# Kernel tuning notes

Measured on AMD Instinct MI355X. Metric: run time of the kernel, lower is better.

The kernel has to match this reference:

```python
import jax, jax.numpy as jnp
import numpy as np

B, T, HID = 2, 4096, 1024
NH, DK, DV = 8, 128, 128
CONV_K = 4
CHUNK = 64


def short_conv_silu(x, w):
    # causal depthwise conv1d, x: [B,T,D], w: [D,K]
    K = w.shape[1]
    xp = jnp.pad(x, ((0, 0), (K - 1, 0), (0, 0)))
    out = sum(xp[:, i:i + x.shape[1], :] * w[:, i] for i in range(K))
    return jax.nn.silu(out)


def hadamard_fm(x, w1, b1, w2, b2):
    # per-head feature map: Linear(x)*Linear(x), x: [B,T,H,D]
    return (jnp.einsum('bthd,ed->bthe', x, w1) + b1) * (jnp.einsum('bthd,ed->bthe', x, w2) + b2)


def chunk_linear_attn(q, k, v, scale):
    # causal linear attention via chunked scan. q,k,v: [B,T,H,D]
    Bq, Tq, H, Dk = q.shape
    Dv = v.shape[-1]
    nc = Tq // CHUNK
    q = (q * scale).reshape(Bq, nc, CHUNK, H, Dk).transpose(1, 0, 2, 3, 4)
    k = k.reshape(Bq, nc, CHUNK, H, Dk).transpose(1, 0, 2, 3, 4)
    v = v.reshape(Bq, nc, CHUNK, H, Dv).transpose(1, 0, 2, 3, 4)
    mask = jnp.tril(jnp.ones((CHUNK, CHUNK), dtype=bool))

    def step(S, inp):
        qc, kc, vc = inp  # [B,C,H,D]
        attn = jnp.einsum('bihk,bjhk->bhij', qc, kc)
        attn = jnp.where(mask, attn, 0.0)
        o = jnp.einsum('bhij,bjhv->bihv', attn, vc) + jnp.einsum('bihk,bhkv->bihv', qc, S)
        S = S + jnp.einsum('bihk,bihv->bhkv', kc, vc)
        return S, o

    S0 = jnp.zeros((Bq, H, Dk, Dv), q.dtype)
    _, o = jax.lax.scan(step, S0, (q, k, v))  # o: [nc,B,C,H,Dv]
    return o.transpose(1, 0, 2, 3, 4).reshape(Bq, Tq, H, Dv)


def setup_inputs() -> dict:
    key = jax.random.key(0)
    ks = jax.random.split(key, 16)
    s = 0.02
    inp = {
        'hidden_states': jax.random.normal(ks[0], (B, T, HID), jnp.float32),
        'wq': jax.random.normal(ks[1], (HID, HID), jnp.float32) * s,
        'wk': jax.random.normal(ks[2], (HID, HID), jnp.float32) * s,
        'wv': jax.random.normal(ks[3], (HID, HID), jnp.float32) * s,
        'wo': jax.random.normal(ks[4], (HID, HID), jnp.float32) * s,
        'conv_q': jax.random.normal(ks[5], (HID, CONV_K), jnp.float32) * 0.2,
        'conv_k': jax.random.normal(ks[6], (HID, CONV_K), jnp.float32) * 0.2,
        'conv_v': jax.random.normal(ks[7], (HID, CONV_K), jnp.float32) * 0.2,
        'fmq_w1': jax.random.normal(ks[8], (DK, DK), jnp.float32) * s,
        'fmq_b1': jnp.zeros((DK,), jnp.float32),
        'fmq_w2': jax.random.normal(ks[9], (DK, DK), jnp.float32) * s,
        'fmq_b2': jnp.zeros((DK,), jnp.float32),
        'fmk_w1': jax.random.normal(ks[10], (DK, DK), jnp.float32) * s,
        'fmk_b1': jnp.zeros((DK,), jnp.float32),
        'fmk_w2': jax.random.normal(ks[11], (DK, DK), jnp.float32) * s,
        'fmk_b2': jnp.zeros((DK,), jnp.float32),
    }
    return inp


def reference(hidden_states, wq, wk, wv, wo, conv_q, conv_k, conv_v,
              fmq_w1, fmq_b1, fmq_w2, fmq_b2, fmk_w1, fmk_b1, fmk_w2, fmk_b2):
    q = short_conv_silu(hidden_states @ wq.T, conv_q)
    k = short_conv_silu(hidden_states @ wk.T, conv_k)
    v = short_conv_silu(hidden_states @ wv.T, conv_v)
    q = q.reshape(B, T, NH, DK)
    k = k.reshape(B, T, NH, DK)
    v = v.reshape(B, T, NH, DV)
    q = hadamard_fm(q, fmq_w1, fmq_b1, fmq_w2, fmq_b2)
    k = hadamard_fm(k, fmk_w1, fmk_b1, fmk_w2, fmk_b2)
    scale = DK ** -0.5
    o = chunk_linear_attn(q, k, v, scale)
    return o.reshape(B, T, NH * DV) @ wo.T
```

## Files before the change

### kernel.cpp

```cpp
#include <hip/hip_runtime.h>
#include <cstdint>
#include <cstddef>

#define T_SEQ 4096
#define BATCH 2
#define HIDDEN 1024
#define NHEAD 8
#define DKV 128
#define BT (BATCH * T_SEQ)
#define NCH 64
#define CHUNK_L 64
#define QSCALE 0.08838834764831845f
#define SCALE_P 1024.0f
#define SCALE_O 8192.0f
#define OEPS 0.7071067811865476f

typedef _Float16 half8 __attribute__((ext_vector_type(8)));
typedef float floatx4 __attribute__((ext_vector_type(4)));

union HBits { _Float16 h; unsigned short u; };

__global__ void cast_f32_f16(const float* __restrict__ X, _Float16* __restrict__ Y, int n8)
{
    int idx = blockIdx.x * 256 + threadIdx.x;
    if (idx < n8) {
        float4 a = ((const float4*)X)[idx * 2];
        float4 b = ((const float4*)X)[idx * 2 + 1];
        half8 h = { (_Float16)a.x, (_Float16)a.y, (_Float16)a.z, (_Float16)a.w,
                    (_Float16)b.x, (_Float16)b.y, (_Float16)b.z, (_Float16)b.w };
        *(half8*)&Y[idx * 8] = h;
    }
}

__global__ void cast8_f32_f16(const float* __restrict__ s0, const float* __restrict__ s1,
                              const float* __restrict__ s2, const float* __restrict__ s3,
                              const float* __restrict__ s4, const float* __restrict__ s5,
                              const float* __restrict__ s6, const float* __restrict__ s7,
                              _Float16* __restrict__ d0, _Float16* __restrict__ d1,
                              _Float16* __restrict__ d2, _Float16* __restrict__ d3,
                              _Float16* __restrict__ d4, _Float16* __restrict__ d5,
                              _Float16* __restrict__ d6, _Float16* __restrict__ d7,
                              int nbig, int nsmall)
{
    int sel = blockIdx.y;
    const float* src; _Float16* dst; int n8;
    switch (sel) {
        case 0: src = s0; dst = d0; n8 = nbig; break;
        case 1: src = s1; dst = d1; n8 = nbig; break;
        case 2: src = s2; dst = d2; n8 = nbig; break;
        case 3: src = s3; dst = d3; n8 = nbig; break;
        case 4: src = s4; dst = d4; n8 = nsmall; break;
        case 5: src = s5; dst = d5; n8 = nsmall; break;
        case 6: src = s6; dst = d6; n8 = nsmall; break;
        default: src = s7; dst = d7; n8 = nsmall; break;
    }
    int idx = blockIdx.x * 256 + threadIdx.x;
    if (idx < n8) {
        float4 u = ((const float4*)src)[idx * 2];
        float4 v = ((const float4*)src)[idx * 2 + 1];
        half8 h = { (_Float16)u.x, (_Float16)u.y, (_Float16)u.z, (_Float16)u.w,
                    (_Float16)v.x, (_Float16)v.y, (_Float16)v.z, (_Float16)v.w };
        *(half8*)&dst[idx * 8] = h;
    }
}

__global__ __launch_bounds__(256) void gemm_nt_f16_h16(const _Float16* __restrict__ A,
                                                       const _Float16* __restrict__ W,
                                                       _Float16* __restrict__ C,
                                                       int M, int N, int K)
{
    __shared__ _Float16 As[128 * 64];
    __shared__ _Float16 Ws[128 * 64];
    const int bm = blockIdx.y * 128;
    const int bn = blockIdx.x * 128;
    const int tid = threadIdx.x;
    const int w = tid >> 6;
    const int l = tid & 63;
    const int wm = (w >> 1) * 64;
    const int wn = (w & 1) * 64;
    const int lane16 = l & 15;
    const int quad = l >> 4;
    const int srow = w * 8 + (l >> 3);
    const int skh = ((l & 7) ^ (l >> 3)) * 8;
    const int rsw = lane16 & 7;

    floatx4 acc[4][4];
#pragma unroll
    for (int i = 0; i < 4; ++i)
#pragma unroll
        for (int j = 0; j < 4; ++j)
            acc[i][j] = (floatx4){0.f, 0.f, 0.f, 0.f};

    for (int k0 = 0; k0 < K; k0 += 64) {
#pragma unroll
        for (int c = 0; c < 4; ++c) {
            int row = c * 32 + srow;
            const _Float16* ga = A + (size_t)(bm + row) * K + k0 + skh;
            const _Float16* gw = W + (size_t)(bn + row) * K + k0 + skh;
            __builtin_amdgcn_global_load_lds(
                (const __attribute__((address_space(1))) void*)ga,
                (__attribute__((address_space(3))) void*)(As + c * 2048 + w * 512), 16, 0, 0);
            __builtin_amdgcn_global_load_lds(
                (const __attribute__((address_space(1))) void*)gw,
                (__attribute__((address_space(3))) void*)(Ws + c * 2048 + w * 512), 16, 0, 0);
        }
        __syncthreads();

#pragma unroll
        for (int s = 0; s < 2; ++s) {
            const int pc = (((s * 4 + quad) ^ rsw)) * 8;
            half8 a[4], b[4];
#pragma unroll
            for (int i = 0; i < 4; ++i) {
                a[i] = *(const half8*)&As[(wm + i * 16 + lane16) * 64 + pc];
                b[i] = *(const half8*)&Ws[(wn + i * 16 + lane16) * 64 + pc];
            }
#pragma unroll
            for (int i = 0; i < 4; ++i)
#pragma unroll
                for (int j = 0; j < 4; ++j)
                    acc[i][j] = __builtin_amdgcn_mfma_f32_16x16x32_f16(a[i], b[j], acc[i][j], 0, 0, 0);
        }
        __syncthreads();
    }
#pragma unroll
    for (int i = 0; i < 4; ++i)
#pragma unroll
        for (int j = 0; j < 4; ++j)
#pragma unroll
            for (int r = 0; r < 4; ++r)
                C[(size_t)(bm + wm + i * 16 + quad * 4 + r) * N + bn + wn + j * 16 + lane16] =
                    (_Float16)acc[i][j][r];
}

__global__ __launch_bounds__(256) void gemm_nt_f16_f32(const _Float16* __restrict__ A,
                                                       const _Float16* __restrict__ W,
                                                       float* __restrict__ C,
                                                       int M, int N, int K, float scale)
{
    __shared__ _Float16 As[128 * 64];
    __shared__ _Float16 Ws[128 * 64];
    const int bm = blockIdx.y * 128;
    const int bn = blockIdx.x * 128;
    const int tid = threadIdx.x;
    const int w = tid >> 6;
    const int l = tid & 63;
    const int wm = (w >> 1) * 64;
    const int wn = (w & 1) * 64;
    const int lane16 = l & 15;
    const int quad = l >> 4;
    const int srow = w * 8 + (l >> 3);
    const int skh = ((l & 7) ^ (l >> 3)) * 8;
    const int rsw = lane16 & 7;

    floatx4 acc[4][4];
#pragma unroll
    for (int i = 0; i < 4; ++i)
#pragma unroll
        for (int j = 0; j < 4; ++j)
            acc[i][j] = (floatx4){0.f, 0.f, 0.f, 0.f};

    for (int k0 = 0; k0 < K; k0 += 64) {
#pragma unroll
        for (int c = 0; c < 4; ++c) {
            int row = c * 32 + srow;
            const _Float16* ga = A + (size_t)(bm + row) * K + k0 + skh;
            const _Float16* gw = W + (size_t)(bn + row) * K + k0 + skh;
            __builtin_amdgcn_global_load_lds(
                (const __attribute__((address_space(1))) void*)ga,
                (__attribute__((address_space(3))) void*)(As + c * 2048 + w * 512), 16, 0, 0);
            __builtin_amdgcn_global_load_lds(
                (const __attribute__((address_space(1))) void*)gw,
                (__attribute__((address_space(3))) void*)(Ws + c * 2048 + w * 512), 16, 0, 0);
        }
        __syncthreads();

#pragma unroll
        for (int s = 0; s < 2; ++s) {
            const int pc = (((s * 4 + quad) ^ rsw)) * 8;
            half8 a[4], b[4];
#pragma unroll
            for (int i = 0; i < 4; ++i) {
                a[i] = *(const half8*)&As[(wm + i * 16 + lane16) * 64 + pc];
                b[i] = *(const half8*)&Ws[(wn + i * 16 + lane16) * 64 + pc];
            }
#pragma unroll
            for (int i = 0; i < 4; ++i)
#pragma unroll
                for (int j = 0; j < 4; ++j)
                    acc[i][j] = __builtin_amdgcn_mfma_f32_16x16x32_f16(a[i], b[j], acc[i][j], 0, 0, 0);
        }
        __syncthreads();
    }
#pragma unroll
    for (int i = 0; i < 4; ++i)
#pragma unroll
        for (int j = 0; j < 4; ++j)
#pragma unroll
            for (int r = 0; r < 4; ++r)
                C[(size_t)(bm + wm + i * 16 + quad * 4 + r) * N + bn + wn + j * 16 + lane16] =
                    acc[i][j][r] * scale;
}

__global__ __launch_bounds__(256) void conv_silu_T(const _Float16* __restrict__ X, int ldx,
                                                   const float* __restrict__ Wc,
                                                   _Float16* __restrict__ VT)
{
    __shared__ _Float16 xs[67 * 64];
    const int bx = blockIdx.x;
    const int t0 = (bx & 63) * 64;
    const int dt = ((bx >> 6) & 15) * 64;
    const int z = bx >> 10;
    const int tid = threadIdx.x;

#pragma unroll
    for (int i = 0; i < 3; ++i) {
        int p = tid + 256 * i;
        if (p < 536) {
            int row = p >> 3, d8 = (p & 7) * 8;
            int t = t0 - 3 + row;
            half8 v;
            if (t >= 0)
                v = *(const half8*)&X[((size_t)z * T_SEQ + t) * ldx + dt + d8];
            else
                v = (half8){0, 0, 0, 0, 0, 0, 0, 0};
            *(half8*)&xs[row * 64 + d8] = v;
        }
    }
    __syncthreads();

    const int d = tid & 63;
    const int dg = dt + d;
    float4 w = *(const float4*)&Wc[dg * 4];
#pragma unroll
    for (int u = 0; u < 2; ++u) {
        int tg = (tid >> 6) + u * 4;
        half8 o;
#pragma unroll
        for (int s = 0; s < 8; ++s) {
            int base = (tg * 8 + s + 3) * 64 + d;
            float acc = (float)xs[base] * w.w
                      + (float)xs[base - 64] * w.z
                      + (float)xs[base - 128] * w.y
                      + (float)xs[base - 192] * w.x;
            o[s] = (_Float16)(acc / (1.f + __expf(-acc)));
        }
        *(half8*)&VT[((size_t)z * HIDDEN + dg) * T_SEQ + t0 + tg * 8] = o;
    }
}

#define XIN_LD 136
__global__ __launch_bounds__(256) void convfm(const _Float16* __restrict__ QKV, int ldx,
                                              const float* __restrict__ Wcq,
                                              const float* __restrict__ Wck,
                                              const _Float16* __restrict__ Wfm,
                                              const float* __restrict__ Bq1,
                                              const float* __restrict__ Bq2,
                                              const float* __restrict__ Bk1,
                                              const float* __restrict__ Bk2,
                                              _Float16* __restrict__ OUTq,
                                              _Float16* __restrict__ OUTk)
{
    const int sel = blockIdx.z;
    const float* Wc = sel ? Wck : Wcq;
    const _Float16* W1h = Wfm + (sel ? 2 * 16384 : 0);
    const _Float16* W2h = Wfm + (sel ? 3 * 16384 : 16384);
    const float* B1 = sel ? Bk1 : Bq1;
    const float* B2 = sel ? Bk2 : Bq2;
    _Float16* OUT = sel ? OUTk : OUTq;

    __shared__ _Float16 xin[67 * XIN_LD];
    __shared__ _Float16 xs[4 * 64 * 32];
    const int t0 = blockIdx.x * 64;
    const int h = blockIdx.y;
    const int tid = threadIdx.x;
    const int w = tid >> 6;
    const int l = tid & 63;
    const int lane16 = l & 15;
    const int quad = l >> 4;
    const bool batch_start = (t0 & (T_SEQ - 1)) == 0;

    for (int p = tid; p < 67 * 16; p += 256) {
        int row = p >> 4, cg = p & 15;
        half8 v;
        if (batch_start && row < 3)
            v = (half8){0, 0, 0, 0, 0, 0, 0, 0};
        else
            v = *(const half8*)&QKV[(size_t)(t0 - 3 + row) * ldx + sel * HIDDEN + h * DKV + cg * 8];
        *(half8*)&xin[row * XIN_LD + cg * 8] = v;
    }
    __syncthreads();

    {
        const int doct = tid & 15;
        const int d0 = doct * 8;
        const int rq = (tid >> 4) * 4;
        const int u = doct >> 2;
        const int col = d0 & 31;

        float w0[8], w1[8], w2[8], w3[8];
#pragma unroll
        for (int e = 0; e < 8; ++e) {
            float4 wv = *(const float4*)&Wc[(h * DKV + d0 + e) * 4];
            w0[e] = wv.x; w1[e] = wv.y; w2[e] = wv.z; w3[e] = wv.w;
        }

#pragma unroll
        for (int rr = 0; rr < 4; ++rr) {
            const int row = rq + rr;
            half8 x3 = *(const half8*)&xin[(row + 0) * XIN_LD + d0];
            half8 x2 = *(const half8*)&xin[(row + 1) * XIN_LD + d0];
            half8 x1 = *(const half8*)&xin[(row + 2) * XIN_LD + d0];
            half8 x0 = *(const half8*)&xin[(row + 3) * XIN_LD + d0];
            half8 o;
#pragma unroll
            for (int e = 0; e < 8; ++e) {
                float acc = fmaf((float)x0[e], w3[e],
                            fmaf((float)x1[e], w2[e],
                            fmaf((float)x2[e], w1[e], (float)x3[e] * w0[e])));
                o[e] = (_Float16)(acc / (1.f + __expf(-acc)));
            }
            *(half8*)&xs[u * 2048 + row * 32 + col] = o;
        }
    }
    __syncthreads();

    floatx4 acc1[4][2], acc2[4][2];
#pragma unroll
    for (int i = 0; i < 4; ++i)
#pragma unroll
        for (int j = 0; j < 2; ++j) {
            acc1[i][j] = (floatx4){0.f, 0.f, 0.f, 0.f};
            acc2[i][j] = (floatx4){0.f, 0.f, 0.f, 0.f};
        }

#pragma unroll
    for (int s = 0; s < 4; ++s) {
        half8 a[4];
#pragma unroll
        for (int mt = 0; mt < 4; ++mt)
            a[mt] = *(const half8*)&xs[s * 2048 + (mt * 16 + lane16) * 32 + quad * 8];
#pragma unroll
        for (int nt = 0; nt < 2; ++nt) {
            int e = w * 32 + nt * 16 + lane16;
            half8 b1 = *(const half8*)&W1h[(size_t)e * DKV + s * 32 + quad * 8];
            half8 b2 = *(const half8*)&W2h[(size_t)e * DKV + s * 32 + quad * 8];
#pragma unroll
            for (int mt = 0; mt < 4; ++mt) {
                acc1[mt][nt] = __builtin_amdgcn_mfma_f32_16x16x32_f16(a[mt], b1, acc1[mt][nt], 0, 0, 0);
                acc2[mt][nt] = __builtin_amdgcn_mfma_f32_16x16x32_f16(a[mt], b2, acc2[mt][nt], 0, 0, 0);
            }
        }
    }

#pragma unroll
    for (int nt = 0; nt < 2; ++nt) {
        int e = w * 32 + nt * 16 + lane16;
        float b1v = B1[e], b2v = B2[e];
#pragma unroll
        for (int mt = 0; mt < 4; ++mt)
#pragma unroll
            for (int r = 0; r < 4; ++r) {
                float o = (acc1[mt][nt][r] + b1v) * (acc2[mt][nt][r] + b2v);
                OUT[(size_t)(t0 + mt * 16 + quad * 4 + r) * HIDDEN + h * DKV + e] = (_Float16)o;
            }
    }
}

__global__ __launch_bounds__(256) void ktv_mfma(const _Float16* __restrict__ Kf,
                                                const _Float16* __restrict__ VT,
                                                _Float16* __restrict__ G16)
{
    __shared__ _Float16 kt[128 * 72];
    const int c = blockIdx.x;
    const int bh = blockIdx.y;
    const int b = bh >> 3, h = bh & 7;
    const int tid = threadIdx.x;
    const int w = tid >> 6;
    const int l = tid & 63;
    const int lane16 = l & 15;
    const int quad = l >> 4;
    const size_t rowbase = (size_t)b * T_SEQ + (size_t)c * CHUNK_L;

    {
        const int dk0 = (tid >> 4) * 8;
        const int jb = (tid & 15) * 4;
        half8 r0 = *(const half8*)&Kf[(rowbase + jb + 0) * HIDDEN + h * DKV + dk0];
        half8 r1 = *(const half8*)&Kf[(rowbase + jb + 1) * HIDDEN + h * DKV + dk0];
        half8 r2 = *(const half8*)&Kf[(rowbase + jb + 2) * HIDDEN + h * DKV + dk0];
        half8 r3 = *(const half8*)&Kf[(rowbase + jb + 3) * HIDDEN + h * DKV + dk0];
#pragma unroll
        for (int dk = 0; dk < 8; ++dk) {
            HBits a0, a1, a2, a3;
            a0.h = r0[dk]; a1.h = r1[dk]; a2.h = r2[dk]; a3.h = r3[dk];
            unsigned int lo = ((unsigned int)a1.u << 16) | a0.u;
            unsigned int hi = ((unsigned int)a3.u << 16) | a2.u;
            *(unsigned int*)&kt[(dk0 + dk) * 72 + jb] = lo;
            *(unsigned int*)&kt[(dk0 + dk) * 72 + jb + 2] = hi;
        }
    }
    __syncthreads();

    const int m0 = (w >> 1) * 64;
    const int n0 = (w & 1) * 64;
    floatx4 acc[4][4];
#pragma unroll
    for (int i = 0; i < 4; ++i)
#pragma unroll
        for (int j = 0; j < 4; ++j)
            acc[i][j] = (floatx4){0.f, 0.f, 0.f, 0.f};

#pragma unroll
    for (int s = 0; s < 2; ++s) {
        half8 a[4], bb[4];
#pragma unroll
        for (int mt = 0; mt < 4; ++mt) {
            int dv = m0 + mt * 16 + lane16;
            a[mt] = *(const half8*)&VT[((size_t)bh * DKV + dv) * T_SEQ + c * CHUNK_L + s * 32 + quad * 8];
        }
#pragma unroll
        for (int nt = 0; nt < 4; ++nt)
            bb[nt] = *(const half8*)&kt[(n0 + nt * 16 + lane16) * 72 + s * 32 + quad * 8];
#pragma unroll
        for (int mt = 0; mt < 4; ++mt)
#pragma unroll
            for (int nt = 0; nt < 4; ++nt)
                acc[mt][nt] = __builtin_amdgcn_mfma_f32_16x16x32_f16(a[mt], bb[nt], acc[mt][nt], 0, 0, 0);
    }

    _Float16* Gp = G16 + ((size_t)bh * NCH + c) * (DKV * DKV);
#pragma unroll
    for (int mt = 0; mt < 4; ++mt)
#pragma unroll
        for (int nt = 0; nt < 4; ++nt)
#pragma unroll
            for (int r = 0; r < 4; ++r)
                Gp[(size_t)(m0 + mt * 16 + quad * 4 + r) * DKV + n0 + nt * 16 + lane16] =
                    (_Float16)acc[mt][nt][r];
}

__global__ void prefix_kernel(const _Float16* __restrict__ G16, _Float16* __restrict__ Gh)
{
    int idx = blockIdx.x * 256 + threadIdx.x;
    int bh = idx >> 14;
    int e = idx & 16383;
    const _Float16* p = G16 + (size_t)bh * NCH * 16384 + e;
    _Float16* q = Gh + (size_t)bh * NCH * 16384 + e;
    float run = 0.f;
#pragma unroll
    for (int c = 0; c < NCH; ++c) {
        q[(size_t)c * 16384] = (_Float16)(run * SCALE_P);
        run += (float)p[(size_t)c * 16384];
    }
}

#define PSLD 40
__global__ __launch_bounds__(256) void attn_mfma(const _Float16* __restrict__ Qf,
                                                 const _Float16* __restrict__ Kf,
                                                 const _Float16* __restrict__ VT,
                                                 const _Float16* __restrict__ Gh,
                                                 _Float16* __restrict__ O)
{
    __shared__ _Float16 ps[2 * 64 * PSLD];
    const int c = blockIdx.x;
    const int bh = blockIdx.y;
    const int b = bh >> 3, h = bh & 7;
    const int tid = threadIdx.x;
    const int w = tid >> 6;
    const int l = tid & 63;
    const int lane16 = l & 15;
    const int quad = l >> 4;
    const size_t rowbase = (size_t)b * T_SEQ + (size_t)c * CHUNK_L;

    {
        const int m0 = (w >> 1) * 32;
        const int n0 = (w & 1) * 32;
        floatx4 aq[2][2];
#pragma unroll
        for (int i = 0; i < 2; ++i)
#pragma unroll
            for (int j = 0; j < 2; ++j)
                aq[i][j] = (floatx4){0.f, 0.f, 0.f, 0.f};
#pragma unroll
        for (int s = 0; s < 4; ++s) {
            half8 a[2], bb[2];
#pragma unroll
            for (int mt = 0; mt < 2; ++mt)
                a[mt] = *(const half8*)&Qf[(rowbase + m0 + mt * 16 + lane16) * HIDDEN +
                                           h * DKV + s * 32 + quad * 8];
#pragma unroll
            for (int nt = 0; nt < 2; ++nt)
                bb[nt] = *(const half8*)&Kf[(rowbase + n0 + nt * 16 + lane16) * HIDDEN +
                                            h * DKV + s * 32 + quad * 8];
#pragma unroll
            for (int mt = 0; mt < 2; ++mt)
#pragma unroll
                for (int nt = 0; nt < 2; ++nt)
                    aq[mt][nt] = __builtin_amdgcn_mfma_f32_16x16x32_f16(a[mt], bb[nt], aq[mt][nt], 0, 0, 0);
        }
#pragma unroll
        for (int mt = 0; mt < 2; ++mt)
#pragma unroll
            for (int nt = 0; nt < 2; ++nt) {
                int j = n0 + nt * 16 + lane16;
#pragma unroll
                for (int r = 0; r < 4; ++r) {
                    int i = m0 + mt * 16 + quad * 4 + r;
                    float v = (j <= i) ? aq[mt][nt][r] * SCALE_P : 0.f;
                    ps[(j >> 5) * 64 * PSLD + i * PSLD + (j & 31)] = (_Float16)v;
                }
            }
    }
    __syncthreads();

    const int n0o = w * 32;
    floatx4 accO[4][2];
#pragma unroll
    for (int i = 0; i < 4; ++i)
#pragma unroll
        for (int j = 0; j < 2; ++j)
            accO[i][j] = (floatx4){0.f, 0.f, 0.f, 0.f};

#pragma unroll
    for (int s = 0; s < 2; ++s) {
        half8 a[4], bb[2];
#pragma unroll
        for (int mt = 0; mt < 4; ++mt)
            a[mt] = *(const half8*)&ps[s * 64 * PSLD + (mt * 16 + lane16) * PSLD + quad * 8];
#pragma unroll
        for (int nt = 0; nt < 2; ++nt) {
            int dv = n0o + nt * 16 + lane16;
            bb[nt] = *(const half8*)&VT[((size_t)bh * DKV + dv) * T_SEQ + c * CHUNK_L + s * 32 + quad * 8];
        }
#pragma unroll
        for (int mt = 0; mt < 4; ++mt)
#pragma unroll
            for (int nt = 0; nt < 2; ++nt)
                accO[mt][nt] = __builtin_amdgcn_mfma_f32_16x16x32_f16(a[mt], bb[nt], accO[mt][nt], 0, 0, 0);
    }

    const _Float16* gh = Gh + ((size_t)bh * NCH + c) * (DKV * DKV);
#pragma unroll
    for (int s = 0; s < 4; ++s) {
        half8 a[4], bb[2];
#pragma unroll
        for (int mt = 0; mt < 4; ++mt)
            a[mt] = *(const half8*)&Qf[(rowbase + mt * 16 + lane16) * HIDDEN +
                                       h * DKV + s * 32 + quad * 8];
#pragma unroll
        for (int nt = 0; nt < 2; ++nt) {
            int dv = n0o + nt * 16 + lane16;
            bb[nt] = *(const half8*)&gh[(size_t)dv * DKV + s * 32 + quad * 8];
        }
#pragma unroll
        for (int mt = 0; mt < 4; ++mt)
#pragma unroll
            for (int nt = 0; nt < 2; ++nt)
                accO[mt][nt] = __builtin_amdgcn_mfma_f32_16x16x32_f16(a[mt], bb[nt], accO[mt][nt], 0, 0, 0);
    }

#pragma unroll
    for (int mt = 0; mt < 4; ++mt)
#pragma unroll
        for (int nt = 0; nt < 2; ++nt)
#pragma unroll
            for (int r = 0; r < 4; ++r)
                O[(rowbase + mt * 16 + quad * 4 + r) * HIDDEN + h * DKV + n0o + nt * 16 + lane16] =
                    (_Float16)(accO[mt][nt][r] * OEPS);
}

extern "C" void kernel_launch(void* const* d_in, const int* in_sizes, int n_in,
                              void* d_out, int out_size, void* d_ws, size_t ws_size,
                              hipStream_t stream)
{
    (void)in_sizes; (void)n_in; (void)out_size; (void)ws_size;
    const float* hs = (const float*)d_in[0];
    const float* wq = (const float*)d_in[1];
    const float* wk = (const float*)d_in[2];
    const float* wv = (const float*)d_in[3];
    const float* wo = (const float*)d_in[4];
    const float* cq = (const float*)d_in[5];
    const float* ck = (const float*)d_in[6];
    const float* cv = (const float*)d_in[7];
    const float* fmq_w1 = (const float*)d_in[8];
    const float* fmq_b1 = (const float*)d_in[9];
    const float* fmq_w2 = (const float*)d_in[10];
    const float* fmq_b2 = (const float*)d_in[11];
    const float* fmk_w1 = (const float*)d_in[12];
    const float* fmk_b1 = (const float*)d_in[13];
    const float* fmk_w2 = (const float*)d_in[14];
    const float* fmk_b2 = (const float*)d_in[15];
    float* out = (float*)d_out;
    char* ws = (char*)d_ws;

    const size_t MB = 1024 * 1024;
    _Float16* h16     = (_Float16*)(ws + 0);
    _Float16* qf16    = (_Float16*)(ws + 0);
    _Float16* wqkv16  = (_Float16*)(ws + 16 * MB);
    _Float16* wo16    = wqkv16 + (3 << 20);
    _Float16* fmw     = wqkv16 + (4 << 20);
    _Float16* qkvlin  = (_Float16*)(ws + 32 * MB);
    _Float16* kf16    = (_Float16*)(ws + 80 * MB);
    _Float16* vT      = (_Float16*)(ws + 96 * MB);
    _Float16* O16     = (_Float16*)(ws + 112 * MB);
    _Float16* G16     = (_Float16*)(ws + 128 * MB);
    _Float16* Gh      = (_Float16*)(ws + 160 * MB);

    cast_f32_f16<<<4096, 256, 0, stream>>>(hs, h16, BT * HIDDEN / 8);
    cast8_f32_f16<<<dim3(512, 8), 256, 0, stream>>>(
        wq, wk, wv, wo, fmq_w1, fmq_w2, fmk_w1, fmk_w2,
        wqkv16, wqkv16 + (1 << 20), wqkv16 + (2 << 20), wo16,
        fmw, fmw + 16384, fmw + 2 * 16384, fmw + 3 * 16384,
        HIDDEN * HIDDEN / 8, DKV * DKV / 8);

    dim3 gqkv(3 * HIDDEN / 128, BT / 128);
    gemm_nt_f16_h16<<<gqkv, 256, 0, stream>>>(h16, wqkv16, qkvlin, BT, 3 * HIDDEN, HIDDEN);

    conv_silu_T<<<2048, 256, 0, stream>>>(qkvlin + 2 * HIDDEN, 3 * HIDDEN, cv, vT);

    dim3 fg(BT / 64, NHEAD, 2);
    convfm<<<fg, 256, 0, stream>>>(qkvlin, 3 * HIDDEN, cq, ck, fmw,
                                   fmq_b1, fmq_b2, fmk_b1, fmk_b2, qf16, kf16);

    dim3 ag(NCH, BATCH * NHEAD);
    ktv_mfma<<<ag, 256, 0, stream>>>(kf16, vT, G16);
    prefix_kernel<<<(16 * 16384) / 256, 256, 0, stream>>>(G16, Gh);
    attn_mfma<<<ag, 256, 0, stream>>>(qf16, kf16, vT, Gh, O16);

    dim3 gg(HIDDEN / 128, BT / 128);
    gemm_nt_f16_f32<<<gg, 256, 0, stream>>>(O16, wo16, out, BT, HIDDEN, HIDDEN, 1.0f / SCALE_O);
}
```

Baseline: 327.0 us.

## Rewrite QKV GEMM as 256x256 tile with double-buffered async LDS pipeline

Replaces the 128x128 single-buffered QKV projection GEMM with a 256x256-tile, 512-thread kernel. The new kernel double-buffers A and W in LDS, interleaves async global-to-LDS loads for the next k-tiles with MFMA compute in four phases, and raises wave priority around the MFMA bursts. The aim is to hide global load latency and raise arithmetic intensity per block. In exchange it uses more LDS and registers and relies on hand-placed waitcnt/barrier sequencing, which is fragile. The grid shrinks to 12x32 blocks, which may underfill the CUs.

```diff
diff --git a/kernel.cpp b/kernel.cpp
--- a/kernel.cpp
+++ b/kernel.cpp
@@ -64,73 +64,168 @@
     }
 }
 
-__global__ __launch_bounds__(256) void gemm_nt_f16_h16(const _Float16* __restrict__ A,
-                                                       const _Float16* __restrict__ W,
-                                                       _Float16* __restrict__ C,
-                                                       int M, int N, int K)
-{
-    __shared__ _Float16 As[128 * 64];
-    __shared__ _Float16 Ws[128 * 64];
-    const int bm = blockIdx.y * 128;
-    const int bn = blockIdx.x * 128;
+#define TILEH 16384
+
+__global__ __launch_bounds__(512, 2) void gemm256_nt_f16_h16(
+    const _Float16* __restrict__ A, const _Float16* __restrict__ W,
+    _Float16* __restrict__ C, int M, int N, int K)
+{
+    __shared__ _Float16 As[2 * TILEH];
+    __shared__ _Float16 Ws[2 * TILEH];
+    const int bm = blockIdx.y * 256;
+    const int bn = blockIdx.x * 256;
     const int tid = threadIdx.x;
     const int w = tid >> 6;
     const int l = tid & 63;
-    const int wm = (w >> 1) * 64;
-    const int wn = (w & 1) * 64;
     const int lane16 = l & 15;
     const int quad = l >> 4;
-    const int srow = w * 8 + (l >> 3);
-    const int skh = ((l & 7) ^ (l >> 3)) * 8;
-    const int rsw = lane16 & 7;
-
-    floatx4 acc[4][4];
-#pragma unroll
-    for (int i = 0; i < 4; ++i)
+    const int wr = w >> 2;
+    const int wc = w & 3;
+    const int NT = K >> 6;
+
+    const int srow = tid >> 3;
+    const int sch = (tid & 7) ^ (srow & 7);
+
+#define STAGE(src, baseRow, k0, q, dst)                                           \
+    __builtin_amdgcn_global_load_lds(                                             \
+        (const __attribute__((address_space(1))) void*)((src) +                   \
+            (size_t)((baseRow) + (q) * 64 + srow) * K + (k0) + sch * 8),          \
+        (__attribute__((address_space(3))) void*)((dst) + (q) * 4096 + w * 512),  \
+        16, 0, 0)
+
+    floatx4 acc[8][4];
+#pragma unroll
+    for (int i = 0; i < 8; ++i)
 #pragma unroll
         for (int j = 0; j < 4; ++j)
             acc[i][j] = (floatx4){0.f, 0.f, 0.f, 0.f};
 
-    for (int k0 = 0; k0 < K; k0 += 64) {
-#pragma unroll
-        for (int c = 0; c < 4; ++c) {
-            int row = c * 32 + srow;
-            const _Float16* ga = A + (size_t)(bm + row) * K + k0 + skh;
-            const _Float16* gw = W + (size_t)(bn + row) * K + k0 + skh;
-            __builtin_amdgcn_global_load_lds(
-                (const __attribute__((address_space(1))) void*)ga,
-                (__attribute__((address_space(3))) void*)(As + c * 2048 + w * 512), 16, 0, 0);
-            __builtin_amdgcn_global_load_lds(
-                (const __attribute__((address_space(1))) void*)gw,
-                (__attribute__((address_space(3))) void*)(Ws + c * 2048 + w * 512), 16, 0, 0);
-        }
-        __syncthreads();
-
-#pragma unroll
-        for (int s = 0; s < 2; ++s) {
-            const int pc = (((s * 4 + quad) ^ rsw)) * 8;
-            half8 a[4], b[4];
-#pragma unroll
-            for (int i = 0; i < 4; ++i) {
-                a[i] = *(const half8*)&As[(wm + i * 16 + lane16) * 64 + pc];
-                b[i] = *(const half8*)&Ws[(wn + i * 16 + lane16) * 64 + pc];
-            }
+    {
+#pragma unroll
+        for (int q = 0; q < 4; ++q) STAGE(W, bn, 0, q, Ws);
+#pragma unroll
+        for (int q = 0; q < 4; ++q) STAGE(A, bm, 0, q, As);
+        if (NT > 1) {
+#pragma unroll
+            for (int q = 0; q < 4; ++q) STAGE(W, bn, 64, q, Ws + TILEH);
+            asm volatile("s_waitcnt vmcnt(4)" ::: "memory");
+        } else {
+            asm volatile("s_waitcnt vmcnt(0)" ::: "memory");
+        }
+        __builtin_amdgcn_s_barrier();
+        asm volatile("" ::: "memory");
+    }
+
+    for (int t = 0; t < NT; ++t) {
+        const int bsel = t & 1;
+        const _Float16* Asb = As + bsel * TILEH;
+        const _Float16* Wsb = Ws + bsel * TILEH;
+        _Float16* AsN = As + (bsel ^ 1) * TILEH;
+        _Float16* WsN = Ws + bsel * TILEH;
+        const int kA = (t + 1) << 6;
+        const int kW = (t + 2) << 6;
+        const bool doA = (t + 1) < NT;
+        const bool doW = (t + 2) < NT;
+
+        half8 a[4][2], b[4][2];
+
+#pragma unroll
+        for (int i = 0; i < 4; ++i)
+#pragma unroll
+            for (int s = 0; s < 2; ++s) {
+                int row = wr * 128 + i * 16 + lane16;
+                a[i][s] = *(const half8*)&Asb[row * 64 + (((s * 4 + quad) ^ (row & 7)) << 3)];
+            }
+#pragma unroll
+        for (int j = 0; j < 2; ++j)
+#pragma unroll
+            for (int s = 0; s < 2; ++s) {
+                int row = wc * 64 + j * 16 + lane16;
+                b[j][s] = *(const half8*)&Wsb[row * 64 + (((s * 4 + quad) ^ (row & 7)) << 3)];
+            }
+        if (doA) { STAGE(A, bm, kA, 0, AsN); STAGE(A, bm, kA, 1, AsN); }
+        asm volatile("s_waitcnt lgkmcnt(8)" ::: "memory");
+        __builtin_amdgcn_s_barrier();
+        asm volatile("s_waitcnt lgkmcnt(0)" ::: "memory");
+        __builtin_amdgcn_s_setprio(1);
+#pragma unroll
+        for (int s = 0; s < 2; ++s)
 #pragma unroll
             for (int i = 0; i < 4; ++i)
 #pragma unroll
-                for (int j = 0; j < 4; ++j)
-                    acc[i][j] = __builtin_amdgcn_mfma_f32_16x16x32_f16(a[i], b[j], acc[i][j], 0, 0, 0);
-        }
-        __syncthreads();
-    }
-#pragma unroll
-    for (int i = 0; i < 4; ++i)
+                for (int j = 0; j < 2; ++j)
+                    acc[i][j] = __builtin_amdgcn_mfma_f32_16x16x32_f16(a[i][s], b[j][s], acc[i][j], 0, 0, 0);
+        __builtin_amdgcn_s_setprio(0);
+        __builtin_amdgcn_s_barrier();
+
+#pragma unroll
+        for (int j = 2; j < 4; ++j)
+#pragma unroll
+            for (int s = 0; s < 2; ++s) {
+                int row = wc * 64 + j * 16 + lane16;
+                b[j][s] = *(const half8*)&Wsb[row * 64 + (((s * 4 + quad) ^ (row & 7)) << 3)];
+            }
+        if (doA) { STAGE(A, bm, kA, 2, AsN); STAGE(A, bm, kA, 3, AsN); }
+        __builtin_amdgcn_s_barrier();
+        asm volatile("s_waitcnt lgkmcnt(0)" ::: "memory");
+        __builtin_amdgcn_s_setprio(1);
+#pragma unroll
+        for (int s = 0; s < 2; ++s)
+#pragma unroll
+            for (int i = 0; i < 4; ++i)
+#pragma unroll
+                for (int j = 2; j < 4; ++j)
+                    acc[i][j] = __builtin_amdgcn_mfma_f32_16x16x32_f16(a[i][s], b[j][s], acc[i][j], 0, 0, 0);
+        __builtin_amdgcn_s_setprio(0);
+        __builtin_amdgcn_s_barrier();
+
+#pragma unroll
+        for (int i = 0; i < 4; ++i)
+#pragma unroll
+            for (int s = 0; s < 2; ++s) {
+                int row = wr * 128 + 64 + i * 16 + lane16;
+                a[i][s] = *(const half8*)&Asb[row * 64 + (((s * 4 + quad) ^ (row & 7)) << 3)];
+            }
+        if (doW) { STAGE(W, bn, kW, 0, WsN); STAGE(W, bn, kW, 1, WsN); }
+        __builtin_amdgcn_s_barrier();
+        asm volatile("s_waitcnt lgkmcnt(0)" ::: "memory");
+        __builtin_amdgcn_s_setprio(1);
+#pragma unroll
+        for (int s = 0; s < 2; ++s)
+#pragma unroll
+            for (int i = 0; i < 4; ++i)
+#pragma unroll
+                for (int j = 0; j < 2; ++j)
+                    acc[4 + i][j] = __builtin_amdgcn_mfma_f32_16x16x32_f16(a[i][s], b[j][s], acc[4 + i][j], 0, 0, 0);
+        __builtin_amdgcn_s_setprio(0);
+        __builtin_amdgcn_s_barrier();
+
+        if (doW) { STAGE(W, bn, kW, 2, WsN); STAGE(W, bn, kW, 3, WsN); }
+        __builtin_amdgcn_s_barrier();
+        __builtin_amdgcn_s_setprio(1);
+#pragma unroll
+        for (int s = 0; s < 2; ++s)
+#pragma unroll
+            for (int i = 0; i < 4; ++i)
+#pragma unroll
+                for (int j = 2; j < 4; ++j)
+                    acc[4 + i][j] = __builtin_amdgcn_mfma_f32_16x16x32_f16(a[i][s], b[j][s], acc[4 + i][j], 0, 0, 0);
+        __builtin_amdgcn_s_setprio(0);
+        if (doW)      asm volatile("s_waitcnt vmcnt(4)" ::: "memory");
+        else if (doA) asm volatile("s_waitcnt vmcnt(0)" ::: "memory");
+        __builtin_amdgcn_s_barrier();
+        asm volatile("" ::: "memory");
+    }
+#undef STAGE
+
+#pragma unroll
+    for (int i = 0; i < 8; ++i)
 #pragma unroll
         for (int j = 0; j < 4; ++j)
 #pragma unroll
             for (int r = 0; r < 4; ++r)
-                C[(size_t)(bm + wm + i * 16 + quad * 4 + r) * N + bn + wn + j * 16 + lane16] =
-                    (_Float16)acc[i][j][r];
+                C[(size_t)(bm + wr * 128 + i * 16 + quad * 4 + r) * N +
+                  bn + wc * 64 + j * 16 + lane16] = (_Float16)acc[i][j][r];
 }
 
 __global__ __launch_bounds__(256) void gemm_nt_f16_f32(const _Float16* __restrict__ A,
@@ -613,8 +708,8 @@
         fmw, fmw + 16384, fmw + 2 * 16384, fmw + 3 * 16384,
         HIDDEN * HIDDEN / 8, DKV * DKV / 8);
 
-    dim3 gqkv(3 * HIDDEN / 128, BT / 128);
-    gemm_nt_f16_h16<<<gqkv, 256, 0, stream>>>(h16, wqkv16, qkvlin, BT, 3 * HIDDEN, HIDDEN);
+    dim3 gqkv(3 * HIDDEN / 256, BT / 256);
+    gemm256_nt_f16_h16<<<gqkv, 512, 0, stream>>>(h16, wqkv16, qkvlin, BT, 3 * HIDDEN, HIDDEN);
 
     conv_silu_T<<<2048, 256, 0, stream>>>(qkvlin + 2 * HIDDEN, 3 * HIDDEN, cv, vT);
 
```

Result: no change. 321.7 us (-1.6%).
